# Kernel optimization log

Measured on AMD Instinct MI355X. Metric: run time of the kernel, lower is better.

The kernel has to match this reference:

```python
import jax, jax.numpy as jnp
import numpy as np

N_STATES, N_OBS = 64, 32
N_TRAJ, T = 128, 250
ALPHA, BETA, KAPPA = 1.0, 2.0, -1.0
DT = 0.02
LAM = ALPHA ** 2 * (N_STATES + KAPPA) - N_STATES  # Merwe scaling lambda


def _weights(n):
    c = 0.5 / (n + LAM)
    Wm = jnp.full((2 * n + 1,), c, dtype=jnp.float32).at[0].set(LAM / (n + LAM))
    Wc = Wm.at[0].add(1.0 - ALPHA ** 2 + BETA)
    return Wm, Wc


def setup_inputs() -> dict:
    key = jax.random.key(0)
    k1, k2, k3, k4 = jax.random.split(key, 4)
    X = jax.random.normal(k1, (N_TRAJ, T, N_STATES), jnp.float32)
    Y = jax.random.normal(k2, (N_TRAJ, T, N_OBS), jnp.float32)
    F = jax.random.normal(k3, (N_STATES, N_STATES), jnp.float32) / np.sqrt(N_STATES)
    H = jax.random.normal(k4, (N_OBS, N_STATES), jnp.float32) / np.sqrt(N_STATES)
    Q = 0.01 * jnp.eye(N_STATES, dtype=jnp.float32)   # q2 * I, as in ctor
    R = 0.01 * jnp.eye(N_OBS, dtype=jnp.float32)      # r2 * I, as in ctor
    return {"X": X, "Y": Y, "F": F, "H": H, "Q": Q, "R": R}


def _sigma_points(x, P):
    # MerweScaledSigmaPoints: rows of upper-triangular chol((n+lam)P) == cols of lower chol
    n = x.shape[0]
    L = jnp.linalg.cholesky((n + LAM) * (P + 1e-8 * jnp.eye(n, dtype=P.dtype)))
    offs = L.T  # (n, n): row i is the i-th sigma offset
    return jnp.concatenate([x[None], x[None] + offs, x[None] - offs], axis=0)  # (2n+1, n)


def _ukf_step(carry, y, F, H, Q, R, Wm, Wc):
    x, P = carry
    # predict: propagate sigma points through fx(x, dt) = x + dt * tanh(F @ x)
    sig = _sigma_points(x, P)                 # (2n+1, n)
    sf = sig + DT * jnp.tanh(sig @ F.T)       # (2n+1, n)
    x_pred = Wm @ sf
    dxs = sf - x_pred
    P_pred = jnp.einsum('k,ki,kj->ij', Wc, dxs, dxs) + Q
    # update: hx(x) = H @ x applied to predicted sigma points (filterpy reuses sigmas_f)
    zs = sf @ H.T                             # (2n+1, m)
    z_pred = Wm @ zs
    dzs = zs - z_pred
    Pz = jnp.einsum('k,ki,kj->ij', Wc, dzs, dzs) + R
    Pxz = jnp.einsum('k,ki,kj->ij', Wc, dxs, dzs)
    K = jnp.linalg.solve(Pz, Pxz.T).T         # Pxz @ inv(Pz)
    x_new = x_pred + K @ (y - z_pred)
    P_new = P_pred - K @ Pz @ K.T
    P_new = 0.5 * (P_new + P_new.T)
    return (x_new, P_new), (x_new, P_new)


def reference(X, Y, F, H, Q, R):
    n = F.shape[0]
    Wm, Wc = _weights(n)

    def run_one(y_seq):
        x0 = jnp.zeros((n,), dtype=Y.dtype)             # ukf.x = zeros
        P0 = 1e-5 * jnp.eye(n, dtype=Y.dtype)           # ukf.P = 1e-5 * I
        step = lambda c, y: _ukf_step(c, y, F, H, Q, R, Wm, Wc)
        _, (xs, Ps) = jax.lax.scan(step, (x0, P0), y_seq)
        return xs, Ps

    traj_estimated, Pk_estimated = jax.vmap(run_one)(Y)  # (N,T,n), (N,T,n,n)
    mse_lin = jnp.mean((traj_estimated - X) ** 2, axis=(1, 2))  # per-traj MSE
    mse_lin_avg = jnp.mean(mse_lin)
    mse_db_avg = 10.0 * jnp.log10(mse_lin_avg)
    return traj_estimated, Pk_estimated, mse_lin_avg, mse_db_avg
```

## Files before the change

kernel.cpp:

```cpp
#include <hip/hip_runtime.h>
#include <math.h>


#define NTRAJ 128
#define TSTEPS 250
#define NS 64
#define NO 32
#define PS 65
#define SFS 68
#define HTS 36
#define PXS 33
#define GJS 65
#define BLK 512

#define DTc 0.02f
#define W_C (0.5f/63.0f)
#define WM0 (-1.0f/63.0f)
#define WC0 (2.0f - 1.0f/63.0f)

__device__ __forceinline__ float tanh_fast(float x) {
  float e = __expf(2.0f * x);
  return 1.0f - 2.0f / (e + 1.0f);
}

__global__ __launch_bounds__(BLK)
void ukf_main(const float* __restrict__ Xg, const float* __restrict__ Yg,
              const float* __restrict__ Fg, const float* __restrict__ Hg,
              const float* __restrict__ Qg, const float* __restrict__ Rg,
              float* __restrict__ outX, float* __restrict__ outP,
              float* __restrict__ wsPart)
{
  __shared__ __align__(16) float P[NS*PS];
  __shared__ __align__(16) float sfb[128*SFS];
  __shared__ __align__(16) float sHT[NS*HTS];
  __shared__ float sPart[8*NS];
  __shared__ float sx[NS], sxp[NS], sFx[NS], s0[NS];
  __shared__ float sinn[NO];

  float* Pxz = sfb;
  float* Km  = sfb + NS*PXS;
  float* Wgj = sfb + 2*NS*PXS;
  float* Mb  = sfb + 2*NS*PXS;

  const int tid  = threadIdx.x;
  const int lane = tid & 63;
  const int grp  = tid >> 6;
  const int traj = blockIdx.x;

  const int pzm = tid >> 4;
  const int pzn = tid & 15;
  const float rv0 = Rg[pzm*NO + pzn];
  const float rv1 = Rg[pzm*NO + pzn + 16];

  for (int o = tid; o < NS*NS; o += BLK) {
    int i = o >> 6, j = o & 63;
    P[i*PS + j] = (i == j) ? (63e-5f + 6.3e-7f) : 0.f;
  }
  for (int o = tid; o < NO*NS; o += BLK) {
    int m = o >> 6, j = o & 63;
    sHT[j*HTS + m] = Hg[o];
  }
  if (tid < NS) sx[tid] = 0.f;
  float errAcc = 0.f;
  __syncthreads();

  for (int t = 0; t < TSTEPS; ++t) {
    const size_t sbase = (size_t)traj*TSTEPS + t;

    for (int pc = 0; pc < NS; pc += 16) {
      if (grp == 0) {
        const int i = lane;
        float pr[16];
        #pragma unroll
        for (int jj = 0; jj < 16; ++jj) pr[jj] = P[i*PS + pc + jj];
        #pragma unroll
        for (int jj = 0; jj < 16; ++jj) {
          const int gc = pc + jj;
          float dv  = __shfl(pr[jj], gc);
          float inv = rsqrtf(dv);
          pr[jj] = (i == gc) ? dv * inv : pr[jj] * inv;
          #pragma unroll
          for (int kk = jj + 1; kk < 16; ++kk) {
            float ck = __shfl(pr[jj], pc + kk);
            pr[kk] = fmaf(-pr[jj], ck, pr[kk]);
          }
        }
        #pragma unroll
        for (int jj = 0; jj < 16; ++jj) P[i*PS + pc + jj] = pr[jj];
      } else if (pc == 0) {
        for (int o = tid - 64; o < NS*NS; o += (BLK - 64)) {
          int i = o >> 6, j = o & 63;
          sfb[j*SFS + i] = Fg[o];
        }
      }
      __syncthreads();
      if (pc < NS - 16) {
        const int i = lane;
        float Li[16];
        #pragma unroll
        for (int jj = 0; jj < 16; ++jj) Li[jj] = P[i*PS + pc + jj];
        for (int k = pc + 16 + grp; k < NS; k += 8) {
          float acc = P[i*PS + k];
          #pragma unroll
          for (int jj = 0; jj < 16; ++jj)
            acc = fmaf(-Li[jj], P[k*PS + pc + jj], acc);
          P[i*PS + k] = acc;
        }
        __syncthreads();
      }
    }

    {
      const int c0 = (tid >> 4) << 1;
      const int j0 = (tid & 15) << 2;
      float a00=0.f,a01=0.f,a02=0.f,a03=0.f, a10=0.f,a11=0.f,a12=0.f,a13=0.f;
      #pragma unroll 2
      for (int jj = 0; jj < NS; ++jj) {
        float4 fv = *(const float4*)&sfb[jj*SFS + j0];
        float lv0 = (jj >= c0)     ? P[jj*PS + c0]     : 0.f;
        float lv1 = (jj >= c0 + 1) ? P[jj*PS + c0 + 1] : 0.f;
        a00 = fmaf(lv0, fv.x, a00); a01 = fmaf(lv0, fv.y, a01);
        a02 = fmaf(lv0, fv.z, a02); a03 = fmaf(lv0, fv.w, a03);
        a10 = fmaf(lv1, fv.x, a10); a11 = fmaf(lv1, fv.y, a11);
        a12 = fmaf(lv1, fv.z, a12); a13 = fmaf(lv1, fv.w, a13);
      }
      float4 w0; w0.x=a00; w0.y=a01; w0.z=a02; w0.w=a03;
      float4 w1; w1.x=a10; w1.y=a11; w1.z=a12; w1.w=a13;
      *(float4*)&sfb[(64 + c0)*SFS + j0]     = w0;
      *(float4*)&sfb[(64 + c0 + 1)*SFS + j0] = w1;
    }
    if (tid < NS) {
      float a2 = 0.f;
      for (int jj = 0; jj < NS; ++jj) a2 = fmaf(sfb[jj*SFS + tid], sx[jj], a2);
      sFx[tid] = a2;
    }
    __syncthreads();

    {
      const int j = lane;
      float psum = 0.f;
      float xv = sx[j], fxv = sFx[j];
      for (int cc = grp; cc < NS; cc += 8) {
        float flv = sfb[(64+cc)*SFS + j];
        float Lv  = (j >= cc) ? P[j*PS + cc] : 0.f;
        float vp = xv + Lv + DTc * tanh_fast(fxv + flv);
        float vm = xv - Lv + DTc * tanh_fast(fxv - flv);
        sfb[cc*SFS + j]      = vp;
        sfb[(64+cc)*SFS + j] = vm;
        psum += vp + vm;
      }
      sPart[grp*NS + j] = psum;
    }
    if (tid < NS) s0[tid] = sx[tid] + DTc * tanh_fast(sFx[tid]);
    __syncthreads();

    if (tid < NS) {
      float s = sPart[tid]        + sPart[NS+tid]   + sPart[2*NS+tid] + sPart[3*NS+tid]
              + sPart[4*NS+tid]   + sPart[5*NS+tid] + sPart[6*NS+tid] + sPart[7*NS+tid];
      float xp = fmaf(W_C, s, WM0 * s0[tid]);
      sxp[tid] = xp;
      s0[tid] -= xp;
    }
    __syncthreads();

    {
      const int i0 = (tid >> 5) << 2;
      const int j0 = (tid & 31) << 1;
      float acc[4][2];
      #pragma unroll
      for (int a = 0; a < 4; ++a) { acc[a][0] = 0.f; acc[a][1] = 0.f; }
      float xi[4];
      #pragma unroll
      for (int a = 0; a < 4; ++a) xi[a] = sxp[i0+a];
      const float xj0 = sxp[j0], xj1 = sxp[j0+1];
      #pragma unroll 4
      for (int r = 0; r < 128; ++r) {
        float4 av = *(const float4*)&sfb[r*SFS + i0];
        float2 bv = *(const float2*)&sfb[r*SFS + j0];
        float db0 = bv.x - xj0, db1 = bv.y - xj1;
        #pragma unroll
        for (int a = 0; a < 4; ++a) {
          float da = ((const float*)&av)[a] - xi[a];
          acc[a][0] = fmaf(da, db0, acc[a][0]);
          acc[a][1] = fmaf(da, db1, acc[a][1]);
        }
      }
      const float d0j0 = s0[j0], d0j1 = s0[j0+1];
      #pragma unroll
      for (int a = 0; a < 4; ++a) {
        float d0a = WC0 * s0[i0+a];
        P[(i0+a)*PS + j0]     = fmaf(d0a, d0j0, W_C * acc[a][0]);
        P[(i0+a)*PS + j0 + 1] = fmaf(d0a, d0j1, W_C * acc[a][1]);
      }
    }
    __syncthreads();

    {
      const int i = lane;
      const int cb = grp * 4;
      float acc0=0.f, acc1=0.f, acc2=0.f, acc3=0.f;
      for (int jj = 0; jj < NS; ++jj) {
        float pv = P[i*PS + jj];
        float4 h = *(const float4*)&sHT[jj*HTS + cb];
        acc0 = fmaf(pv, h.x, acc0); acc1 = fmaf(pv, h.y, acc1);
        acc2 = fmaf(pv, h.z, acc2); acc3 = fmaf(pv, h.w, acc3);
      }
      Pxz[i*PXS + cb]     = acc0;
      Pxz[i*PXS + cb + 1] = acc1;
      Pxz[i*PXS + cb + 2] = acc2;
      Pxz[i*PXS + cb + 3] = acc3;
    }
    __syncthreads();

    {
      float a0 = rv0, a1 = rv1;
      for (int i2 = 0; i2 < NS; ++i2) {
        float hv = sHT[i2*HTS + pzm];
        a0 = fmaf(hv, Pxz[i2*PXS + pzn], a0);
        a1 = fmaf(hv, Pxz[i2*PXS + pzn + 16], a1);
      }
      Wgj[pzm*GJS + pzn]      = a0;
      Wgj[pzm*GJS + pzn + 16] = a1;
    }
    __syncthreads();

    if (grp == 0) {
      const int c = lane;
      float w[NO];
      #pragma unroll
      for (int r = 0; r < NO; ++r)
        w[r] = (c < NO) ? Wgj[r*GJS + c] : ((c - NO == r) ? 1.f : 0.f);
      #pragma unroll
      for (int p = 0; p < NO; ++p) {
        float piv = __shfl(w[p], p);
        float rp  = 1.0f / piv;
        float wp  = w[p] * rp;
        #pragma unroll
        for (int r = 0; r < NO; ++r) {
          if (r == p) continue;
          float cr = __shfl(w[r], p);
          w[r] = fmaf(-cr, wp, w[r]);
        }
        w[p] = wp;
      }
      if (c >= NO) {
        #pragma unroll
        for (int r = 0; r < NO; ++r) Wgj[(c - NO)*PXS + r] = w[r];
      }
    } else if (grp == 1) {
      if (lane < NO) {
        float z = 0.f;
        for (int jj = 0; jj < NS; ++jj) z = fmaf(sHT[jj*HTS + lane], sxp[jj], z);
        sinn[lane] = Yg[sbase*NO + lane] - z;
      }
    } else {
      for (int o = tid - 128; o < NS*NS; o += 6*64) {
        int i = o >> 6, j = o & 63;
        P[i*PS + j] += Qg[o];
      }
    }
    __syncthreads();

    {
      const int i = lane;
      const int cb = grp * 4;
      float acc0=0.f, acc1=0.f, acc2=0.f, acc3=0.f;
      for (int n2 = 0; n2 < NO; ++n2) {
        float pv = Pxz[i*PXS + n2];
        acc0 = fmaf(pv, Wgj[(cb    )*PXS + n2], acc0);
        acc1 = fmaf(pv, Wgj[(cb + 1)*PXS + n2], acc1);
        acc2 = fmaf(pv, Wgj[(cb + 2)*PXS + n2], acc2);
        acc3 = fmaf(pv, Wgj[(cb + 3)*PXS + n2], acc3);
      }
      Km[i*PXS + cb]     = acc0;
      Km[i*PXS + cb + 1] = acc1;
      Km[i*PXS + cb + 2] = acc2;
      Km[i*PXS + cb + 3] = acc3;
    }
    __syncthreads();

    if (tid < 272) {
      int k = (int)((sqrtf(4.f*(float)tid + 1.f) - 1.f) * 0.5f);
      while ((k+1)*(k+2) <= tid) ++k;
      while (k*(k+1) > tid) --k;
      const int r0 = tid - k*(k+1);
      const int rb  = (r0 <= k) ? (2*k) : (2*k + 1);
      const int cb2 = (r0 <= k) ? r0 : (r0 - (k + 1));
      const int i0 = rb << 1, j0 = cb2 << 2;
      float acc[2][4];
      #pragma unroll
      for (int b = 0; b < 4; ++b) { acc[0][b] = 0.f; acc[1][b] = 0.f; }
      for (int m = 0; m < NO; ++m) {
        float ka0 = Km[i0*PXS + m];
        float ka1 = Km[(i0+1)*PXS + m];
        #pragma unroll
        for (int b = 0; b < 4; ++b) {
          float pb = Pxz[(j0+b)*PXS + m];
          acc[0][b] = fmaf(ka0, pb, acc[0][b]);
          acc[1][b] = fmaf(ka1, pb, acc[1][b]);
        }
      }
      #pragma unroll
      for (int b = 0; b < 4; ++b) {
        Mb[i0*GJS + j0 + b]     = acc[0][b];
        Mb[(i0+1)*GJS + j0 + b] = acc[1][b];
      }
    } else if (tid >= 448) {
      const int i = tid - 448;
      float xn = sxp[i];
      #pragma unroll 8
      for (int m = 0; m < NO; ++m) xn = fmaf(Km[i*PXS + m], sinn[m], xn);
      sx[i] = xn;
      outX[sbase*NS + i] = xn;
      float dd = xn - Xg[sbase*NS + i];
      errAcc = fmaf(dd, dd, errAcc);
    }
    __syncthreads();

    for (int o = tid; o < NS*NS; o += BLK) {
      int i = o >> 6, j = o & 63;
      float mv = (i >= j) ? Mb[i*GJS + j] : Mb[j*GJS + i];
      float v = P[i*PS + j] - mv;
      outP[sbase*(size_t)(NS*NS) + o] = v;
      float nv = v * 63.f;
      if (i == j) nv += 6.3e-7f;
      P[i*PS + j] = nv;
    }
    __syncthreads();
  }

  if (grp == 7) {
    float v = errAcc;
    for (int off = 32; off > 0; off >>= 1) v += __shfl_down(v, off);
    if (lane == 0) wsPart[traj] = v;
  }
}

__global__ __launch_bounds__(128)
void mse_reduce(const float* __restrict__ part, float* __restrict__ outS)
{
  __shared__ float sbuf[128];
  int tid = threadIdx.x;
  sbuf[tid] = part[tid];
  __syncthreads();
  if (tid < 64) {
    float v = sbuf[tid] + sbuf[tid + 64];
    for (int off = 32; off > 0; off >>= 1) v += __shfl_down(v, off);
    if (tid == 0) {
      float m = v / (128.f * 250.f * 64.f);
      outS[0] = m;
      outS[1] = 10.f * log10f(m);
    }
  }
}

extern "C" void kernel_launch(void* const* d_in, const int* in_sizes, int n_in,
                              void* d_out, int out_size, void* d_ws, size_t ws_size,
                              hipStream_t stream) {
  const float* Xg = (const float*)d_in[0];
  const float* Yg = (const float*)d_in[1];
  const float* Fg = (const float*)d_in[2];
  const float* Hg = (const float*)d_in[3];
  const float* Qg = (const float*)d_in[4];
  const float* Rg = (const float*)d_in[5];

  float* outX = (float*)d_out;
  float* outP = outX + (size_t)NTRAJ*TSTEPS*NS;
  float* outS = outP + (size_t)NTRAJ*TSTEPS*NS*NS;
  float* wsP  = (float*)d_ws;

  hipLaunchKernelGGL(ukf_main, dim3(NTRAJ), dim3(BLK), 0, stream,
                     Xg, Yg, Fg, Hg, Qg, Rg, outX, outP, wsP);
  hipLaunchKernelGGL(mse_reduce, dim3(1), dim3(128), 0, stream, wsP, outS);
}
```

Baseline: 9.780 ms.

## Restructure UKF step: 32-wide Cholesky panels, overlapped F·L, float4 LDS layouts

Replaces the four 16-column Cholesky panel passes with two 32-column panels and one trailing update, which cuts the number of barriers per step. The first half of the F·L product now runs on the other waves while wave 0 factors the second panel. Sigma deviations are subtracted in place so the covariance GEMM reads them directly. The Kalman gain and P update are reformulated around T = H·P (Pz = T·Hᵀ + R, K = Tᵀ·Pz⁻¹), with padded strides of 68 so float4 LDS accesses line up. The cost is a 32-float register panel per lane, more live registers, and a full (non-symmetric) K·T product written directly to outP.

```diff
diff --git a/kernel.cpp b/kernel.cpp
--- a/kernel.cpp
+++ b/kernel.cpp
@@ -6,21 +6,46 @@
 #define TSTEPS 250
 #define NS 64
 #define NO 32
-#define PS 65
+#define PS 68
 #define SFS 68
 #define HTS 36
-#define PXS 33
-#define GJS 65
+#define TS 68
+#define GJS 68
+#define PZS 36
+#define KTS 68
 #define BLK 512
 
 #define DTc 0.02f
 #define W_C (0.5f/63.0f)
 #define WM0 (-1.0f/63.0f)
 #define WC0 (2.0f - 1.0f/63.0f)
+#define DEPS 6.3e-7f
 
 __device__ __forceinline__ float tanh_fast(float x) {
   float e = __expf(2.0f * x);
   return 1.0f - 2.0f / (e + 1.0f);
+}
+
+__device__ __forceinline__ void chol_panel32(float* P, int pc, int lane) {
+  float pr[32];
+  #pragma unroll
+  for (int c4 = 0; c4 < 8; ++c4)
+    *(float4*)&pr[c4*4] = *(const float4*)&P[lane*PS + pc + c4*4];
+  #pragma unroll
+  for (int jj = 0; jj < 32; ++jj) {
+    const int gc = pc + jj;
+    float dv  = __shfl(pr[jj], gc);
+    float inv = rsqrtf(dv);
+    pr[jj] = (lane == gc) ? dv * inv : ((lane < gc) ? 0.f : pr[jj] * inv);
+    #pragma unroll
+    for (int kk = jj + 1; kk < 32; ++kk) {
+      float ck = __shfl(pr[jj], pc + kk);
+      pr[kk] = fmaf(-pr[jj], ck, pr[kk]);
+    }
+  }
+  #pragma unroll
+  for (int c4 = 0; c4 < 8; ++c4)
+    *(float4*)&P[lane*PS + pc + c4*4] = *(const float4*)&pr[c4*4];
 }
 
 __global__ __launch_bounds__(BLK)
@@ -33,28 +58,27 @@
   __shared__ __align__(16) float P[NS*PS];
   __shared__ __align__(16) float sfb[128*SFS];
   __shared__ __align__(16) float sHT[NS*HTS];
-  __shared__ float sPart[8*NS];
-  __shared__ float sx[NS], sxp[NS], sFx[NS], s0[NS];
-  __shared__ float sinn[NO];
-
-  float* Pxz = sfb;
-  float* Km  = sfb + NS*PXS;
-  float* Wgj = sfb + 2*NS*PXS;
-  float* Mb  = sfb + 2*NS*PXS;
+  __shared__ __align__(16) float sPart[8*NS];
+  __shared__ __align__(16) float sx[NS];
+  __shared__ __align__(16) float sxp[NS];
+  __shared__ __align__(16) float sFx[NS];
+  __shared__ __align__(16) float s0[NS];
+  __shared__ __align__(16) float sd0[NS];
+  __shared__ __align__(16) float sinn[NO];
+
+  float* Tb  = sfb;
+  float* Pzb = sfb + 2176;
+  float* Pzi = sfb + 4352;
+  float* Ktb = sfb + 5504;
 
   const int tid  = threadIdx.x;
   const int lane = tid & 63;
   const int grp  = tid >> 6;
   const int traj = blockIdx.x;
 
-  const int pzm = tid >> 4;
-  const int pzn = tid & 15;
-  const float rv0 = Rg[pzm*NO + pzn];
-  const float rv1 = Rg[pzm*NO + pzn + 16];
-
   for (int o = tid; o < NS*NS; o += BLK) {
     int i = o >> 6, j = o & 63;
-    P[i*PS + j] = (i == j) ? (63e-5f + 6.3e-7f) : 0.f;
+    P[i*PS + j] = (i == j) ? (63e-5f + DEPS) : 0.f;
   }
   for (int o = tid; o < NO*NS; o += BLK) {
     int m = o >> 6, j = o & 63;
@@ -67,72 +91,81 @@
   for (int t = 0; t < TSTEPS; ++t) {
     const size_t sbase = (size_t)traj*TSTEPS + t;
 
-    for (int pc = 0; pc < NS; pc += 16) {
-      if (grp == 0) {
-        const int i = lane;
-        float pr[16];
+    if (grp == 0) {
+      chol_panel32(P, 0, lane);
+    } else {
+      for (int c = tid - 64; c < 1024; c += (BLK - 64)) {
+        int i = c >> 4, j0 = (c & 15) << 2;
+        float4 fv = *(const float4*)&Fg[i*64 + j0];
+        sfb[(j0    )*SFS + i] = fv.x;
+        sfb[(j0 + 1)*SFS + i] = fv.y;
+        sfb[(j0 + 2)*SFS + i] = fv.z;
+        sfb[(j0 + 3)*SFS + i] = fv.w;
+      }
+    }
+    __syncthreads();
+
+    {
+      const int k  = 32 + (lane & 31);
+      const int ib = 32 + grp*2 + (lane >> 5);
+      float Lk[32];
+      #pragma unroll
+      for (int c4 = 0; c4 < 8; ++c4)
+        *(float4*)&Lk[c4*4] = *(const float4*)&P[k*PS + c4*4];
+      #pragma unroll
+      for (int it = 0; it < 2; ++it) {
+        const int i = ib + 16*it;
+        float acc = P[i*PS + k];
         #pragma unroll
-        for (int jj = 0; jj < 16; ++jj) pr[jj] = P[i*PS + pc + jj];
-        #pragma unroll
-        for (int jj = 0; jj < 16; ++jj) {
-          const int gc = pc + jj;
-          float dv  = __shfl(pr[jj], gc);
-          float inv = rsqrtf(dv);
-          pr[jj] = (i == gc) ? dv * inv : pr[jj] * inv;
-          #pragma unroll
-          for (int kk = jj + 1; kk < 16; ++kk) {
-            float ck = __shfl(pr[jj], pc + kk);
-            pr[kk] = fmaf(-pr[jj], ck, pr[kk]);
-          }
+        for (int c4 = 0; c4 < 8; ++c4) {
+          float4 pi = *(const float4*)&P[i*PS + c4*4];
+          acc = fmaf(-pi.x, Lk[c4*4    ], acc);
+          acc = fmaf(-pi.y, Lk[c4*4 + 1], acc);
+          acc = fmaf(-pi.z, Lk[c4*4 + 2], acc);
+          acc = fmaf(-pi.w, Lk[c4*4 + 3], acc);
         }
-        #pragma unroll
-        for (int jj = 0; jj < 16; ++jj) P[i*PS + pc + jj] = pr[jj];
-      } else if (pc == 0) {
-        for (int o = tid - 64; o < NS*NS; o += (BLK - 64)) {
-          int i = o >> 6, j = o & 63;
-          sfb[j*SFS + i] = Fg[o];
+        P[i*PS + k] = acc;
+      }
+    }
+    __syncthreads();
+
+    if (grp == 0) {
+      chol_panel32(P, 32, lane);
+    } else if (grp == 7) {
+      const int i2 = lane;
+      float a2 = 0.f;
+      for (int jj = 0; jj < NS; ++jj) a2 = fmaf(sfb[jj*SFS + i2], sx[jj], a2);
+      sFx[i2] = a2;
+    } else {
+      const int widx = tid - 64;
+      for (int itm = widx; itm < 512; itm += 384) {
+        const int c  = itm >> 4;
+        const int j0 = (itm & 15) << 2;
+        float ax = 0.f, ay = 0.f, az = 0.f, aw = 0.f;
+        for (int jj = 0; jj < NS; ++jj) {
+          float4 fv = *(const float4*)&sfb[jj*SFS + j0];
+          float lv  = P[jj*PS + c];
+          ax = fmaf(lv, fv.x, ax); ay = fmaf(lv, fv.y, ay);
+          az = fmaf(lv, fv.z, az); aw = fmaf(lv, fv.w, aw);
         }
-      }
-      __syncthreads();
-      if (pc < NS - 16) {
-        const int i = lane;
-        float Li[16];
-        #pragma unroll
-        for (int jj = 0; jj < 16; ++jj) Li[jj] = P[i*PS + pc + jj];
-        for (int k = pc + 16 + grp; k < NS; k += 8) {
-          float acc = P[i*PS + k];
-          #pragma unroll
-          for (int jj = 0; jj < 16; ++jj)
-            acc = fmaf(-Li[jj], P[k*PS + pc + jj], acc);
-          P[i*PS + k] = acc;
-        }
-        __syncthreads();
-      }
-    }
-
-    {
-      const int c0 = (tid >> 4) << 1;
+        float4 w4; w4.x = ax; w4.y = ay; w4.z = az; w4.w = aw;
+        *(float4*)&sfb[(64 + c)*SFS + j0] = w4;
+      }
+    }
+    __syncthreads();
+
+    {
+      const int c  = 32 + (tid >> 4);
       const int j0 = (tid & 15) << 2;
-      float a00=0.f,a01=0.f,a02=0.f,a03=0.f, a10=0.f,a11=0.f,a12=0.f,a13=0.f;
-      #pragma unroll 2
-      for (int jj = 0; jj < NS; ++jj) {
+      float ax = 0.f, ay = 0.f, az = 0.f, aw = 0.f;
+      for (int jj = 32; jj < NS; ++jj) {
         float4 fv = *(const float4*)&sfb[jj*SFS + j0];
-        float lv0 = (jj >= c0)     ? P[jj*PS + c0]     : 0.f;
-        float lv1 = (jj >= c0 + 1) ? P[jj*PS + c0 + 1] : 0.f;
-        a00 = fmaf(lv0, fv.x, a00); a01 = fmaf(lv0, fv.y, a01);
-        a02 = fmaf(lv0, fv.z, a02); a03 = fmaf(lv0, fv.w, a03);
-        a10 = fmaf(lv1, fv.x, a10); a11 = fmaf(lv1, fv.y, a11);
-        a12 = fmaf(lv1, fv.z, a12); a13 = fmaf(lv1, fv.w, a13);
-      }
-      float4 w0; w0.x=a00; w0.y=a01; w0.z=a02; w0.w=a03;
-      float4 w1; w1.x=a10; w1.y=a11; w1.z=a12; w1.w=a13;
-      *(float4*)&sfb[(64 + c0)*SFS + j0]     = w0;
-      *(float4*)&sfb[(64 + c0 + 1)*SFS + j0] = w1;
-    }
-    if (tid < NS) {
-      float a2 = 0.f;
-      for (int jj = 0; jj < NS; ++jj) a2 = fmaf(sfb[jj*SFS + tid], sx[jj], a2);
-      sFx[tid] = a2;
+        float lv  = P[jj*PS + c];
+        ax = fmaf(lv, fv.x, ax); ay = fmaf(lv, fv.y, ay);
+        az = fmaf(lv, fv.z, az); aw = fmaf(lv, fv.w, aw);
+      }
+      float4 w4; w4.x = ax; w4.y = ay; w4.z = az; w4.w = aw;
+      *(float4*)&sfb[(64 + c)*SFS + j0] = w4;
     }
     __syncthreads();
 
@@ -141,12 +174,12 @@
       float psum = 0.f;
       float xv = sx[j], fxv = sFx[j];
       for (int cc = grp; cc < NS; cc += 8) {
-        float flv = sfb[(64+cc)*SFS + j];
-        float Lv  = (j >= cc) ? P[j*PS + cc] : 0.f;
+        float flv = sfb[(64 + cc)*SFS + j];
+        float Lv  = P[j*PS + cc];
         float vp = xv + Lv + DTc * tanh_fast(fxv + flv);
         float vm = xv - Lv + DTc * tanh_fast(fxv - flv);
-        sfb[cc*SFS + j]      = vp;
-        sfb[(64+cc)*SFS + j] = vm;
+        sfb[cc*SFS + j]        = vp;
+        sfb[(64 + cc)*SFS + j] = vm;
         psum += vp + vm;
       }
       sPart[grp*NS + j] = psum;
@@ -154,73 +187,91 @@
     if (tid < NS) s0[tid] = sx[tid] + DTc * tanh_fast(sFx[tid]);
     __syncthreads();
 
-    if (tid < NS) {
-      float s = sPart[tid]        + sPart[NS+tid]   + sPart[2*NS+tid] + sPart[3*NS+tid]
-              + sPart[4*NS+tid]   + sPart[5*NS+tid] + sPart[6*NS+tid] + sPart[7*NS+tid];
-      float xp = fmaf(W_C, s, WM0 * s0[tid]);
-      sxp[tid] = xp;
-      s0[tid] -= xp;
-    }
-    __syncthreads();
-
-    {
-      const int i0 = (tid >> 5) << 2;
-      const int j0 = (tid & 31) << 1;
-      float acc[4][2];
-      #pragma unroll
-      for (int a = 0; a < 4; ++a) { acc[a][0] = 0.f; acc[a][1] = 0.f; }
-      float xi[4];
-      #pragma unroll
-      for (int a = 0; a < 4; ++a) xi[a] = sxp[i0+a];
-      const float xj0 = sxp[j0], xj1 = sxp[j0+1];
+    {
+      const int r  = tid >> 4;
+      const int j0 = (tid & 15) << 2;
+      float4 s0r = *(const float4*)&s0[j0];
+      float sx_ = 0.f, sy_ = 0.f, sz_ = 0.f, sw_ = 0.f;
+      #pragma unroll
+      for (int g = 0; g < 8; ++g) {
+        float4 p = *(const float4*)&sPart[g*NS + j0];
+        sx_ += p.x; sy_ += p.y; sz_ += p.z; sw_ += p.w;
+      }
+      float4 xp;
+      xp.x = fmaf(W_C, sx_, WM0 * s0r.x);
+      xp.y = fmaf(W_C, sy_, WM0 * s0r.y);
+      xp.z = fmaf(W_C, sz_, WM0 * s0r.z);
+      xp.w = fmaf(W_C, sw_, WM0 * s0r.w);
+      #pragma unroll
+      for (int q = 0; q < 4; ++q) {
+        const int row = r + (q << 5);
+        float4 v = *(const float4*)&sfb[row*SFS + j0];
+        v.x -= xp.x; v.y -= xp.y; v.z -= xp.z; v.w -= xp.w;
+        *(float4*)&sfb[row*SFS + j0] = v;
+      }
+      if (r == 0) *(float4*)&sxp[j0] = xp;
+      if (r == 1) {
+        float4 d; d.x = s0r.x - xp.x; d.y = s0r.y - xp.y;
+        d.z = s0r.z - xp.z; d.w = s0r.w - xp.w;
+        *(float4*)&sd0[j0] = d;
+      }
+    }
+    __syncthreads();
+
+    {
+      const int i0 = (tid >> 4) << 1;
+      const int j0 = (tid & 15) << 2;
+      float a0x=0.f,a0y=0.f,a0z=0.f,a0w=0.f, a1x=0.f,a1y=0.f,a1z=0.f,a1w=0.f;
       #pragma unroll 4
-      for (int r = 0; r < 128; ++r) {
-        float4 av = *(const float4*)&sfb[r*SFS + i0];
-        float2 bv = *(const float2*)&sfb[r*SFS + j0];
-        float db0 = bv.x - xj0, db1 = bv.y - xj1;
-        #pragma unroll
-        for (int a = 0; a < 4; ++a) {
-          float da = ((const float*)&av)[a] - xi[a];
-          acc[a][0] = fmaf(da, db0, acc[a][0]);
-          acc[a][1] = fmaf(da, db1, acc[a][1]);
-        }
-      }
-      const float d0j0 = s0[j0], d0j1 = s0[j0+1];
-      #pragma unroll
-      for (int a = 0; a < 4; ++a) {
-        float d0a = WC0 * s0[i0+a];
-        P[(i0+a)*PS + j0]     = fmaf(d0a, d0j0, W_C * acc[a][0]);
-        P[(i0+a)*PS + j0 + 1] = fmaf(d0a, d0j1, W_C * acc[a][1]);
-      }
-    }
-    __syncthreads();
-
-    {
-      const int i = lane;
-      const int cb = grp * 4;
-      float acc0=0.f, acc1=0.f, acc2=0.f, acc3=0.f;
+      for (int r2 = 0; r2 < 128; ++r2) {
+        float2 av = *(const float2*)&sfb[r2*SFS + i0];
+        float4 bv = *(const float4*)&sfb[r2*SFS + j0];
+        a0x = fmaf(av.x, bv.x, a0x); a0y = fmaf(av.x, bv.y, a0y);
+        a0z = fmaf(av.x, bv.z, a0z); a0w = fmaf(av.x, bv.w, a0w);
+        a1x = fmaf(av.y, bv.x, a1x); a1y = fmaf(av.y, bv.y, a1y);
+        a1z = fmaf(av.y, bv.z, a1z); a1w = fmaf(av.y, bv.w, a1w);
+      }
+      float2 di = *(const float2*)&sd0[i0];
+      float4 dj = *(const float4*)&sd0[j0];
+      float d0 = WC0 * di.x, d1 = WC0 * di.y;
+      float4 w0, w1;
+      w0.x = fmaf(d0, dj.x, W_C * a0x); w0.y = fmaf(d0, dj.y, W_C * a0y);
+      w0.z = fmaf(d0, dj.z, W_C * a0z); w0.w = fmaf(d0, dj.w, W_C * a0w);
+      w1.x = fmaf(d1, dj.x, W_C * a1x); w1.y = fmaf(d1, dj.y, W_C * a1y);
+      w1.z = fmaf(d1, dj.z, W_C * a1z); w1.w = fmaf(d1, dj.w, W_C * a1w);
+      *(float4*)&P[(i0    )*PS + j0] = w0;
+      *(float4*)&P[(i0 + 1)*PS + j0] = w1;
+    }
+    __syncthreads();
+
+    {
+      const int m  = tid >> 4;
+      const int c0 = (tid & 15) << 2;
+      float ax = 0.f, ay = 0.f, az = 0.f, aw = 0.f;
       for (int jj = 0; jj < NS; ++jj) {
-        float pv = P[i*PS + jj];
-        float4 h = *(const float4*)&sHT[jj*HTS + cb];
-        acc0 = fmaf(pv, h.x, acc0); acc1 = fmaf(pv, h.y, acc1);
-        acc2 = fmaf(pv, h.z, acc2); acc3 = fmaf(pv, h.w, acc3);
-      }
-      Pxz[i*PXS + cb]     = acc0;
-      Pxz[i*PXS + cb + 1] = acc1;
-      Pxz[i*PXS + cb + 2] = acc2;
-      Pxz[i*PXS + cb + 3] = acc3;
-    }
-    __syncthreads();
-
-    {
-      float a0 = rv0, a1 = rv1;
-      for (int i2 = 0; i2 < NS; ++i2) {
-        float hv = sHT[i2*HTS + pzm];
-        a0 = fmaf(hv, Pxz[i2*PXS + pzn], a0);
-        a1 = fmaf(hv, Pxz[i2*PXS + pzn + 16], a1);
-      }
-      Wgj[pzm*GJS + pzn]      = a0;
-      Wgj[pzm*GJS + pzn + 16] = a1;
+        float hv  = sHT[jj*HTS + m];
+        float4 pv = *(const float4*)&P[jj*PS + c0];
+        ax = fmaf(hv, pv.x, ax); ay = fmaf(hv, pv.y, ay);
+        az = fmaf(hv, pv.z, az); aw = fmaf(hv, pv.w, aw);
+      }
+      float4 w4; w4.x = ax; w4.y = ay; w4.z = az; w4.w = aw;
+      *(float4*)&Tb[m*TS + c0] = w4;
+    }
+    __syncthreads();
+
+    {
+      const int m  = tid >> 4;
+      const int n0 = (tid & 15) << 1;
+      float2 rv = *(const float2*)&Rg[m*NO + n0];
+      float a0 = rv.x, a1 = rv.y;
+      for (int jj = 0; jj < NS; ++jj) {
+        float tv  = Tb[m*TS + jj];
+        float2 hv = *(const float2*)&sHT[jj*HTS + n0];
+        a0 = fmaf(tv, hv.x, a0);
+        a1 = fmaf(tv, hv.y, a1);
+      }
+      float2 w2; w2.x = a0; w2.y = a1;
+      *(float2*)&Pzb[m*GJS + n0] = w2;
     }
     __syncthreads();
 
@@ -229,7 +280,7 @@
       float w[NO];
       #pragma unroll
       for (int r = 0; r < NO; ++r)
-        w[r] = (c < NO) ? Wgj[r*GJS + c] : ((c - NO == r) ? 1.f : 0.f);
+        w[r] = (c < NO) ? Pzb[r*GJS + c] : ((c - NO == r) ? 1.f : 0.f);
       #pragma unroll
       for (int p = 0; p < NO; ++p) {
         float piv = __shfl(w[p], p);
@@ -245,7 +296,7 @@
       }
       if (c >= NO) {
         #pragma unroll
-        for (int r = 0; r < NO; ++r) Wgj[(c - NO)*PXS + r] = w[r];
+        for (int r = 0; r < NO; ++r) Pzi[(c - NO)*PZS + r] = w[r];
       }
     } else if (grp == 1) {
       if (lane < NO) {
@@ -254,82 +305,78 @@
         sinn[lane] = Yg[sbase*NO + lane] - z;
       }
     } else {
-      for (int o = tid - 128; o < NS*NS; o += 6*64) {
-        int i = o >> 6, j = o & 63;
-        P[i*PS + j] += Qg[o];
-      }
-    }
-    __syncthreads();
-
-    {
-      const int i = lane;
-      const int cb = grp * 4;
-      float acc0=0.f, acc1=0.f, acc2=0.f, acc3=0.f;
-      for (int n2 = 0; n2 < NO; ++n2) {
-        float pv = Pxz[i*PXS + n2];
-        acc0 = fmaf(pv, Wgj[(cb    )*PXS + n2], acc0);
-        acc1 = fmaf(pv, Wgj[(cb + 1)*PXS + n2], acc1);
-        acc2 = fmaf(pv, Wgj[(cb + 2)*PXS + n2], acc2);
-        acc3 = fmaf(pv, Wgj[(cb + 3)*PXS + n2], acc3);
-      }
-      Km[i*PXS + cb]     = acc0;
-      Km[i*PXS + cb + 1] = acc1;
-      Km[i*PXS + cb + 2] = acc2;
-      Km[i*PXS + cb + 3] = acc3;
-    }
-    __syncthreads();
-
-    if (tid < 272) {
-      int k = (int)((sqrtf(4.f*(float)tid + 1.f) - 1.f) * 0.5f);
-      while ((k+1)*(k+2) <= tid) ++k;
-      while (k*(k+1) > tid) --k;
-      const int r0 = tid - k*(k+1);
-      const int rb  = (r0 <= k) ? (2*k) : (2*k + 1);
-      const int cb2 = (r0 <= k) ? r0 : (r0 - (k + 1));
-      const int i0 = rb << 1, j0 = cb2 << 2;
-      float acc[2][4];
-      #pragma unroll
-      for (int b = 0; b < 4; ++b) { acc[0][b] = 0.f; acc[1][b] = 0.f; }
+      const int idx = tid - 128;
+      for (int it = idx; it < 1024; it += 384) {
+        const int i = it >> 4, j0 = (it & 15) << 2;
+        float4 q = *(const float4*)&Qg[i*64 + j0];
+        float4 p = *(const float4*)&P[i*PS + j0];
+        p.x += q.x; p.y += q.y; p.z += q.z; p.w += q.w;
+        *(float4*)&P[i*PS + j0] = p;
+      }
+    }
+    __syncthreads();
+
+    {
+      const int i0 = (tid & 15) << 2;
+      const int cb = tid >> 4;
+      float ax = 0.f, ay = 0.f, az = 0.f, aw = 0.f;
       for (int m = 0; m < NO; ++m) {
-        float ka0 = Km[i0*PXS + m];
-        float ka1 = Km[(i0+1)*PXS + m];
-        #pragma unroll
-        for (int b = 0; b < 4; ++b) {
-          float pb = Pxz[(j0+b)*PXS + m];
-          acc[0][b] = fmaf(ka0, pb, acc[0][b]);
-          acc[1][b] = fmaf(ka1, pb, acc[1][b]);
-        }
-      }
-      #pragma unroll
-      for (int b = 0; b < 4; ++b) {
-        Mb[i0*GJS + j0 + b]     = acc[0][b];
-        Mb[(i0+1)*GJS + j0 + b] = acc[1][b];
-      }
-    } else if (tid >= 448) {
-      const int i = tid - 448;
+        float4 tv = *(const float4*)&Tb[m*TS + i0];
+        float zv  = Pzi[cb*PZS + m];
+        ax = fmaf(tv.x, zv, ax); ay = fmaf(tv.y, zv, ay);
+        az = fmaf(tv.z, zv, az); aw = fmaf(tv.w, zv, aw);
+      }
+      float4 w4; w4.x = ax; w4.y = ay; w4.z = az; w4.w = aw;
+      *(float4*)&Ktb[cb*KTS + i0] = w4;
+    }
+    __syncthreads();
+
+    {
+      const int i0 = (tid >> 4) << 1;
+      const int j0 = (tid & 15) << 2;
+      float a0x=0.f,a0y=0.f,a0z=0.f,a0w=0.f, a1x=0.f,a1y=0.f,a1z=0.f,a1w=0.f;
+      for (int m = 0; m < NO; ++m) {
+        float2 ka = *(const float2*)&Ktb[m*KTS + i0];
+        float4 tb = *(const float4*)&Tb[m*TS + j0];
+        a0x = fmaf(ka.x, tb.x, a0x); a0y = fmaf(ka.x, tb.y, a0y);
+        a0z = fmaf(ka.x, tb.z, a0z); a0w = fmaf(ka.x, tb.w, a0w);
+        a1x = fmaf(ka.y, tb.x, a1x); a1y = fmaf(ka.y, tb.y, a1y);
+        a1z = fmaf(ka.y, tb.z, a1z); a1w = fmaf(ka.y, tb.w, a1w);
+      }
+      float4 p0 = *(const float4*)&P[(i0    )*PS + j0];
+      float4 p1 = *(const float4*)&P[(i0 + 1)*PS + j0];
+      float4 g0, g1;
+      g0.x = p0.x - a0x; g0.y = p0.y - a0y; g0.z = p0.z - a0z; g0.w = p0.w - a0w;
+      g1.x = p1.x - a1x; g1.y = p1.y - a1y; g1.z = p1.z - a1z; g1.w = p1.w - a1w;
+      float* op = &outP[sbase*(size_t)(NS*NS)];
+      *(float4*)&op[(i0    )*64 + j0] = g0;
+      *(float4*)&op[(i0 + 1)*64 + j0] = g1;
+      float4 s0w, s1w;
+      s0w.x = fmaf(g0.x, 63.f, (i0     == j0    ) ? DEPS : 0.f);
+      s0w.y = fmaf(g0.y, 63.f, (i0     == j0 + 1) ? DEPS : 0.f);
+      s0w.z = fmaf(g0.z, 63.f, (i0     == j0 + 2) ? DEPS : 0.f);
+      s0w.w = fmaf(g0.w, 63.f, (i0     == j0 + 3) ? DEPS : 0.f);
+      s1w.x = fmaf(g1.x, 63.f, (i0 + 1 == j0    ) ? DEPS : 0.f);
+      s1w.y = fmaf(g1.y, 63.f, (i0 + 1 == j0 + 1) ? DEPS : 0.f);
+      s1w.z = fmaf(g1.z, 63.f, (i0 + 1 == j0 + 2) ? DEPS : 0.f);
+      s1w.w = fmaf(g1.w, 63.f, (i0 + 1 == j0 + 3) ? DEPS : 0.f);
+      *(float4*)&P[(i0    )*PS + j0] = s0w;
+      *(float4*)&P[(i0 + 1)*PS + j0] = s1w;
+    }
+    if (tid < NS) {
+      const int i = tid;
       float xn = sxp[i];
       #pragma unroll 8
-      for (int m = 0; m < NO; ++m) xn = fmaf(Km[i*PXS + m], sinn[m], xn);
+      for (int m = 0; m < NO; ++m) xn = fmaf(Ktb[m*KTS + i], sinn[m], xn);
       sx[i] = xn;
       outX[sbase*NS + i] = xn;
       float dd = xn - Xg[sbase*NS + i];
       errAcc = fmaf(dd, dd, errAcc);
     }
     __syncthreads();
-
-    for (int o = tid; o < NS*NS; o += BLK) {
-      int i = o >> 6, j = o & 63;
-      float mv = (i >= j) ? Mb[i*GJS + j] : Mb[j*GJS + i];
-      float v = P[i*PS + j] - mv;
-      outP[sbase*(size_t)(NS*NS) + o] = v;
-      float nv = v * 63.f;
-      if (i == j) nv += 6.3e-7f;
-      P[i*PS + j] = nv;
-    }
-    __syncthreads();
-  }
-
-  if (grp == 7) {
+  }
+
+  if (grp == 0) {
     float v = errAcc;
     for (int off = 32; off > 0; off >>= 1) v += __shfl_down(v, off);
     if (lane == 0) wsPart[traj] = v;
```

Result: slower. 12.03 ms (+23.0%).
